# Performance work log

Measured on AMD Instinct MI355X. Metric: run time of the kernel, lower is better.

## Reference

```python
import jax, jax.numpy as jnp
import numpy as np

B, N, D_IN, D_H, D_OUT = 32768, 8, 256, 512, 256
LN_EPS = 1e-5


def setup_inputs() -> dict:
    key = jax.random.key(0)
    ks = jax.random.split(key, 9)
    s = lambda fan_in: 1.0 / np.sqrt(fan_in)
    return {
        "state": jax.random.normal(ks[0], (B, D_IN), dtype=jnp.float32),
        "neighbor_states": jax.random.normal(ks[1], (N, B, D_IN), dtype=jnp.float32),
        "ln_gamma": jnp.ones((D_IN,), jnp.float32),
        "ln_beta": jnp.zeros((D_IN,), jnp.float32),
        "W1": jax.random.uniform(ks[2], (D_IN, D_H), jnp.float32, -s(D_IN), s(D_IN)),
        "b1": jax.random.uniform(ks[3], (D_H,), jnp.float32, -s(D_IN), s(D_IN)),
        "W2": jax.random.uniform(ks[4], (D_H, D_OUT), jnp.float32, -s(D_H), s(D_H)),
        "b2": jax.random.uniform(ks[5], (D_OUT,), jnp.float32, -s(D_H), s(D_H)),
        "attn_w": jax.random.uniform(ks[6], (D_OUT,), jnp.float32, -s(D_OUT), s(D_OUT)),
        "attn_b": jax.random.uniform(ks[7], (), jnp.float32, -s(D_OUT), s(D_OUT)),
    }


def reference(state, neighbor_states, ln_gamma, ln_beta, W1, b1, W2, b2, attn_w, attn_b):
    def process(x):
        # LayerNorm over last dim (eps=1e-5, elementwise affine)
        mu = jnp.mean(x, axis=-1, keepdims=True)
        var = jnp.mean(jnp.square(x - mu), axis=-1, keepdims=True)
        xn = (x - mu) * jax.lax.rsqrt(var + LN_EPS) * ln_gamma + ln_beta
        # Linear -> (Dropout=identity in eval) -> ReLU -> Linear
        h = jax.nn.relu(xn @ W1 + b1)
        return h @ W2 + b2

    local = process(state)                      # [B, D_OUT]
    nf = process(neighbor_states)               # [N, B, D_OUT]
    # attention aggregation: scores over neighbor axis (torch stacks at dim=1)
    scores = jnp.einsum("nbo,o->nb", nf, attn_w) + attn_b   # [N, B]
    weights = jax.nn.softmax(scores, axis=0)                  # softmax over neighbors
    agg = jnp.einsum("nbo,nb->bo", nf, weights)              # [B, D_OUT]
    return local + agg
```

## Files before the change

kernel.cpp:

```cpp
#include <hip/hip_runtime.h>
#include <hip/hip_bf16.h>
#include <math.h>

#define BROWS 32768
#define NNB   8
#define DIN   256
#define DH    512
#define DOUT  256
#define MTILE 64
#define CH    32
#define NCHUNK 16
#define SA    264
#define SH    40

typedef __attribute__((ext_vector_type(8))) short bfrag;
typedef __attribute__((ext_vector_type(4))) float ffrag;
typedef __attribute__((ext_vector_type(4))) short s4v;

__device__ __forceinline__ short f2bf(float f) {
    union { float f; unsigned u; } v; v.f = f;
    unsigned r = v.u + 0x7fffu + ((v.u >> 16) & 1u);
    return (short)(r >> 16);
}

__global__ void tcast(const float* __restrict__ src, short* __restrict__ dst,
                      int R, int C) {
    __shared__ short t[64][67];
    const int c0 = blockIdx.x * 64, r0 = blockIdx.y * 64;
    const int lr = threadIdx.x >> 6, lc = threadIdx.x & 63;
    #pragma unroll
    for (int i = 0; i < 16; ++i) {
        int row = i * 4 + lr;
        t[row][lc] = f2bf(src[(size_t)(r0 + row) * C + c0 + lc]);
    }
    __syncthreads();
    #pragma unroll
    for (int i = 0; i < 16; ++i) {
        int row = i * 4 + lr;
        dst[(size_t)(c0 + row) * R + r0 + lc] = t[lc][row];
    }
}

__global__ __launch_bounds__(256, 2)
void fused_node(const float* __restrict__ state, const float* __restrict__ nbr,
                const float* __restrict__ gamma, const float* __restrict__ beta,
                const float* __restrict__ b1g, const float* __restrict__ b2g,
                const float* __restrict__ awg, const float* __restrict__ abg,
                const short* __restrict__ w1t, const short* __restrict__ w2t,
                float* __restrict__ out) {
    __shared__ short xn_lds[MTILE * SA];
    __shared__ short w1_lds[CH * SA];
    __shared__ short w2_lds[DOUT * SH];
    __shared__ short h_lds[MTILE * SH];
    __shared__ float g_lds[DIN], bt_lds[DIN];
    __shared__ float scorep[4 * MTILE];
    __shared__ float m_lds[MTILE], l_lds[MTILE], al_lds[MTILE], pp_lds[MTILE], il_lds[MTILE];

    const int tid = threadIdx.x;
    const int wv = tid >> 6, lane = tid & 63;
    const int q = lane >> 4, l16 = lane & 15;
    const int row0 = blockIdx.x * MTILE;
    const int cb = wv * 64;

    g_lds[tid] = gamma[tid];
    bt_lds[tid] = beta[tid];
    if (tid < MTILE) { m_lds[tid] = -__builtin_huge_valf(); l_lds[tid] = 0.f; }

    float b2v[4], awv[4];
    #pragma unroll
    for (int ct = 0; ct < 4; ++ct) {
        int col = cb + ct * 16 + l16;
        b2v[ct] = b2g[col];
        awv[ct] = awg[col];
    }
    const float attnb = abg[0];

    ffrag agg[4][4];
    #pragma unroll
    for (int mt = 0; mt < 4; ++mt)
        #pragma unroll
        for (int ct = 0; ct < 4; ++ct) {
            ffrag z = {0.f, 0.f, 0.f, 0.f};
            agg[mt][ct] = z;
        }

    ffrag feat[4][4];

    for (int s = 0; s < 9; ++s) {
        const bool loc = (s == 8);
        const float* xb = loc ? (state + (size_t)row0 * DIN)
                              : (nbr + ((size_t)s * BROWS + (size_t)row0) * DIN);
        __syncthreads();
        {
            const int r = tid >> 2, qq = tid & 3;
            const float* src = xb + r * DIN + qq * 64;
            float s0 = 0.f, s1 = 0.f, q0 = 0.f, q1 = 0.f;
            #pragma unroll
            for (int i = 0; i < 16; ++i) {
                float4 v = ((const float4*)src)[i];
                s0 += v.x + v.y;
                s1 += v.z + v.w;
                q0 = fmaf(v.x, v.x, fmaf(v.y, v.y, q0));
                q1 = fmaf(v.z, v.z, fmaf(v.w, v.w, q1));
            }
            float sum = s0 + s1, ssq = q0 + q1;
            sum += __shfl_xor(sum, 1); sum += __shfl_xor(sum, 2);
            ssq += __shfl_xor(ssq, 1); ssq += __shfl_xor(ssq, 2);
            float mean = sum * (1.f / 256.f);
            float var = ssq * (1.f / 256.f) - mean * mean;
            float rstd = rsqrtf(var + 1e-5f);
            short* dst = xn_lds + r * SA + qq * 64;
            #pragma unroll
            for (int i = 0; i < 16; ++i) {
                float4 v = ((const float4*)src)[i];
                int c = qq * 64 + i * 4;
                float4 g4 = *(const float4*)(g_lds + c);
                float4 t4 = *(const float4*)(bt_lds + c);
                s4v t;
                t.x = f2bf(fmaf((v.x - mean) * rstd, g4.x, t4.x));
                t.y = f2bf(fmaf((v.y - mean) * rstd, g4.y, t4.y));
                t.z = f2bf(fmaf((v.z - mean) * rstd, g4.z, t4.z));
                t.w = f2bf(fmaf((v.w - mean) * rstd, g4.w, t4.w));
                *(s4v*)(dst + i * 4) = t;
            }
        }
        #pragma unroll
        for (int mt = 0; mt < 4; ++mt)
            #pragma unroll
            for (int ct = 0; ct < 4; ++ct) {
                ffrag fi = {b2v[ct], b2v[ct], b2v[ct], b2v[ct]};
                feat[mt][ct] = fi;
            }

        for (int c = 0; c < NCHUNK; ++c) {
            __syncthreads();
            {
                const short* s1 = w1t + c * CH * DIN;
                #pragma unroll
                for (int i = 0; i < 4; ++i) {
                    int f = tid + 256 * i;
                    int rr = f >> 5, c8 = f & 31;
                    *(bfrag*)(w1_lds + rr * SA + c8 * 8) = *(const bfrag*)(s1 + f * 8);
                }
                const short* s2 = w2t + c * CH;
                #pragma unroll
                for (int i = 0; i < 4; ++i) {
                    int f = tid + 256 * i;
                    int rr = f >> 2, c8 = f & 3;
                    *(bfrag*)(w2_lds + rr * SH + c8 * 8) = *(const bfrag*)(s2 + rr * DH + c8 * 8);
                }
            }
            __syncthreads();
            {
                float bb0 = b1g[c * CH + l16], bb1 = b1g[c * CH + 16 + l16];
                ffrag h0 = {bb0, bb0, bb0, bb0};
                ffrag h1 = {bb1, bb1, bb1, bb1};
                const short* ap  = xn_lds + (wv * 16 + l16) * SA + q * 8;
                const short* bp0 = w1_lds + l16 * SA + q * 8;
                const short* bp1 = w1_lds + (16 + l16) * SA + q * 8;
                #pragma unroll
                for (int kb = 0; kb < 8; ++kb) {
                    bfrag a  = *(const bfrag*)(ap + kb * 32);
                    bfrag v0 = *(const bfrag*)(bp0 + kb * 32);
                    bfrag v1 = *(const bfrag*)(bp1 + kb * 32);
                    h0 = __builtin_amdgcn_mfma_f32_16x16x32_bf16(a, v0, h0, 0, 0, 0);
                    h1 = __builtin_amdgcn_mfma_f32_16x16x32_bf16(a, v1, h1, 0, 0, 0);
                }
                short* hb = h_lds + (wv * 16 + q * 4) * SH + l16;
                #pragma unroll
                for (int r = 0; r < 4; ++r) {
                    hb[r * SH]      = f2bf(fmaxf(h0[r], 0.f));
                    hb[r * SH + 16] = f2bf(fmaxf(h1[r], 0.f));
                }
            }
            __syncthreads();
            {
                bfrag af[4], bf[4];
                #pragma unroll
                for (int mt = 0; mt < 4; ++mt)
                    af[mt] = *(const bfrag*)(h_lds + (mt * 16 + l16) * SH + q * 8);
                #pragma unroll
                for (int ct = 0; ct < 4; ++ct)
                    bf[ct] = *(const bfrag*)(w2_lds + (cb + ct * 16 + l16) * SH + q * 8);
                #pragma unroll
                for (int mt = 0; mt < 4; ++mt)
                    #pragma unroll
                    for (int ct = 0; ct < 4; ++ct)
                        feat[mt][ct] = __builtin_amdgcn_mfma_f32_16x16x32_bf16(af[mt], bf[ct], feat[mt][ct], 0, 0, 0);
            }
        }

        if (!loc) {
            float sp[4][4];
            #pragma unroll
            for (int mt = 0; mt < 4; ++mt)
                #pragma unroll
                for (int r = 0; r < 4; ++r) {
                    float vv = feat[mt][0][r] * awv[0] + feat[mt][1][r] * awv[1]
                             + feat[mt][2][r] * awv[2] + feat[mt][3][r] * awv[3];
                    vv += __shfl_xor(vv, 1); vv += __shfl_xor(vv, 2);
                    vv += __shfl_xor(vv, 4); vv += __shfl_xor(vv, 8);
                    sp[mt][r] = vv;
                }
            if (l16 == 0) {
                #pragma unroll
                for (int mt = 0; mt < 4; ++mt)
                    #pragma unroll
                    for (int r = 0; r < 4; ++r)
                        scorep[wv * MTILE + mt * 16 + q * 4 + r] = sp[mt][r];
            }
            __syncthreads();
            if (tid < MTILE) {
                float sc = scorep[tid] + scorep[MTILE + tid] + scorep[2 * MTILE + tid]
                         + scorep[3 * MTILE + tid] + attnb;
                float mo = m_lds[tid];
                float mn = fmaxf(mo, sc);
                float al = __expf(mo - mn);
                float pp = __expf(sc - mn);
                float ln = l_lds[tid] * al + pp;
                m_lds[tid] = mn; l_lds[tid] = ln;
                al_lds[tid] = al; pp_lds[tid] = pp;
                if (s == NNB - 1) il_lds[tid] = 1.f / ln;
            }
            __syncthreads();
            #pragma unroll
            for (int mt = 0; mt < 4; ++mt) {
                float alv[4], ppv[4];
                #pragma unroll
                for (int r = 0; r < 4; ++r) {
                    int rr = mt * 16 + q * 4 + r;
                    alv[r] = al_lds[rr]; ppv[r] = pp_lds[rr];
                }
                #pragma unroll
                for (int ct = 0; ct < 4; ++ct)
                    #pragma unroll
                    for (int r = 0; r < 4; ++r)
                        agg[mt][ct][r] = agg[mt][ct][r] * alv[r] + ppv[r] * feat[mt][ct][r];
            }
        }
    }

    #pragma unroll
    for (int mt = 0; mt < 4; ++mt)
        #pragma unroll
        for (int r = 0; r < 4; ++r) {
            int rr = mt * 16 + q * 4 + r;
            float il = il_lds[rr];
            size_t base = (size_t)(row0 + rr) * DOUT + cb + l16;
            #pragma unroll
            for (int ct = 0; ct < 4; ++ct)
                out[base + ct * 16] = feat[mt][ct][r] + agg[mt][ct][r] * il;
        }
}

extern "C" void kernel_launch(void* const* d_in, const int* in_sizes, int n_in,
                              void* d_out, int out_size, void* d_ws, size_t ws_size,
                              hipStream_t stream) {
    const float* state = (const float*)d_in[0];
    const float* nbr   = (const float*)d_in[1];
    const float* gamma = (const float*)d_in[2];
    const float* beta  = (const float*)d_in[3];
    const float* W1    = (const float*)d_in[4];
    const float* b1    = (const float*)d_in[5];
    const float* W2    = (const float*)d_in[6];
    const float* b2    = (const float*)d_in[7];
    const float* aw    = (const float*)d_in[8];
    const float* ab    = (const float*)d_in[9];
    float* out = (float*)d_out;

    short* w1t = (short*)d_ws;
    short* w2t = w1t + (size_t)DH * DIN;

    tcast<<<dim3(DH / 64, DIN / 64), 256, 0, stream>>>(W1, w1t, DIN, DH);
    tcast<<<dim3(DOUT / 64, DH / 64), 256, 0, stream>>>(W2, w2t, DH, DOUT);
    fused_node<<<BROWS / MTILE, 256, 0, stream>>>(state, nbr, gamma, beta,
                                                  b1, b2, aw, ab, w1t, w2t, out);
}
```

Measured before the change: 723.2 us.

## Double-buffer weight chunks, fold LayerNorm affine into W1, keep xn in registers

Folds the LayerNorm gamma into W1 and beta into a precomputed b1, which removes the affine work from the hot loop. The normalized activations now live in registers as MFMA A-fragments instead of LDS. The block grows to 512 threads and 128 rows, and W1/W2 chunks are double-buffered with register prefetch to overlap global loads with compute and remove one barrier per chunk. Nontemporal loads and stores are added for the streaming activations and output. In exchange the kernel uses more registers per thread and launches a few extra small kernels.

Result: faster. 635.4 us (-12.1%).

```diff
diff --git a/kernel.cpp b/kernel.cpp
--- a/kernel.cpp
+++ b/kernel.cpp
@@ -7,7 +7,7 @@
 #define DIN   256
 #define DH    512
 #define DOUT  256
-#define MTILE 64
+#define MROWS 128
 #define CH    32
 #define NCHUNK 16
 #define SA    264
@@ -15,12 +15,30 @@
 
 typedef __attribute__((ext_vector_type(8))) short bfrag;
 typedef __attribute__((ext_vector_type(4))) float ffrag;
-typedef __attribute__((ext_vector_type(4))) short s4v;
+typedef __attribute__((ext_vector_type(4))) float f4v;
 
 __device__ __forceinline__ short f2bf(float f) {
     union { float f; unsigned u; } v; v.f = f;
     unsigned r = v.u + 0x7fffu + ((v.u >> 16) & 1u);
     return (short)(r >> 16);
+}
+
+__global__ void tcast_g(const float* __restrict__ src, const float* __restrict__ g,
+                        short* __restrict__ dst, int R, int C) {
+    __shared__ short t[64][67];
+    const int c0 = blockIdx.x * 64, r0 = blockIdx.y * 64;
+    const int lr = threadIdx.x >> 6, lc = threadIdx.x & 63;
+    #pragma unroll
+    for (int i = 0; i < 16; ++i) {
+        int row = i * 4 + lr;
+        t[row][lc] = f2bf(src[(size_t)(r0 + row) * C + c0 + lc] * g[r0 + row]);
+    }
+    __syncthreads();
+    #pragma unroll
+    for (int i = 0; i < 16; ++i) {
+        int row = i * 4 + lr;
+        dst[(size_t)(c0 + row) * R + r0 + lc] = t[lc][row];
+    }
 }
 
 __global__ void tcast(const float* __restrict__ src, short* __restrict__ dst,
@@ -41,35 +59,53 @@
     }
 }
 
-__global__ __launch_bounds__(256, 2)
+__global__ void b1prep(const float* __restrict__ W1, const float* __restrict__ b1,
+                       const float* __restrict__ beta, float* __restrict__ b1p) {
+    int n = blockIdx.x * 256 + threadIdx.x;
+    float acc = b1[n];
+    for (int k = 0; k < DIN; ++k) acc += beta[k] * W1[(size_t)k * DH + n];
+    b1p[n] = acc;
+}
+
+__global__ __launch_bounds__(512, 2)
 void fused_node(const float* __restrict__ state, const float* __restrict__ nbr,
-                const float* __restrict__ gamma, const float* __restrict__ beta,
-                const float* __restrict__ b1g, const float* __restrict__ b2g,
+                const float* __restrict__ b1p, const float* __restrict__ b2g,
                 const float* __restrict__ awg, const float* __restrict__ abg,
                 const short* __restrict__ w1t, const short* __restrict__ w2t,
                 float* __restrict__ out) {
-    __shared__ short xn_lds[MTILE * SA];
-    __shared__ short w1_lds[CH * SA];
-    __shared__ short w2_lds[DOUT * SH];
-    __shared__ short h_lds[MTILE * SH];
-    __shared__ float g_lds[DIN], bt_lds[DIN];
-    __shared__ float scorep[4 * MTILE];
-    __shared__ float m_lds[MTILE], l_lds[MTILE], al_lds[MTILE], pp_lds[MTILE], il_lds[MTILE];
+    __shared__ short w1_lds[2][CH * SA];
+    __shared__ short w2_lds[2][DOUT * SH];
+    __shared__ short h_lds[MROWS * SH];
+    __shared__ float b1_lds[DH];
+    __shared__ float scorep[4 * MROWS];
+    __shared__ float m_lds[MROWS], l_lds[MROWS], al_lds[MROWS], pp_lds[MROWS], il_lds[MROWS];
 
     const int tid = threadIdx.x;
     const int wv = tid >> 6, lane = tid & 63;
     const int q = lane >> 4, l16 = lane & 15;
-    const int row0 = blockIdx.x * MTILE;
-    const int cb = wv * 64;
-
-    g_lds[tid] = gamma[tid];
-    bt_lds[tid] = beta[tid];
-    if (tid < MTILE) { m_lds[tid] = -__builtin_huge_valf(); l_lds[tid] = 0.f; }
+    const int rg = wv >> 2, cg = wv & 3;
+    const int row0 = blockIdx.x * MROWS;
+    const int myrow = 16 * wv + l16;
+
+    const int f0 = tid, f1 = tid + 512;
+    const int w1r0 = f0 >> 5, w1c0 = f0 & 31, w1r1 = f1 >> 5, w1c1 = f1 & 31;
+    const int w2r0 = f0 >> 2, w2c0 = f0 & 3,  w2r1 = f1 >> 2, w2c1 = f1 & 3;
+
+    bfrag L1a = *(const bfrag*)(w1t + (size_t)f0 * 8);
+    bfrag L1b = *(const bfrag*)(w1t + (size_t)f1 * 8);
+    bfrag L2a = *(const bfrag*)(w2t + (size_t)w2r0 * DH + w2c0 * 8);
+    bfrag L2b = *(const bfrag*)(w2t + (size_t)w2r1 * DH + w2c1 * 8);
+    if (tid < DH) b1_lds[tid] = b1p[tid];
+    if (tid < MROWS) { m_lds[tid] = -__builtin_huge_valf(); l_lds[tid] = 0.f; }
+    *(bfrag*)(&w1_lds[0][w1r0 * SA + w1c0 * 8]) = L1a;
+    *(bfrag*)(&w1_lds[0][w1r1 * SA + w1c1 * 8]) = L1b;
+    *(bfrag*)(&w2_lds[0][w2r0 * SH + w2c0 * 8]) = L2a;
+    *(bfrag*)(&w2_lds[0][w2r1 * SH + w2c1 * 8]) = L2b;
 
     float b2v[4], awv[4];
     #pragma unroll
     for (int ct = 0; ct < 4; ++ct) {
-        int col = cb + ct * 16 + l16;
+        int col = 64 * cg + 16 * ct + l16;
         b2v[ct] = b2g[col];
         awv[ct] = awg[col];
     }
@@ -79,49 +115,46 @@
     #pragma unroll
     for (int mt = 0; mt < 4; ++mt)
         #pragma unroll
-        for (int ct = 0; ct < 4; ++ct) {
-            ffrag z = {0.f, 0.f, 0.f, 0.f};
-            agg[mt][ct] = z;
-        }
+        for (int ct = 0; ct < 4; ++ct) { ffrag z = {0.f,0.f,0.f,0.f}; agg[mt][ct] = z; }
 
     ffrag feat[4][4];
+    bfrag xnf[8];
 
     for (int s = 0; s < 9; ++s) {
         const bool loc = (s == 8);
         const float* xb = loc ? (state + (size_t)row0 * DIN)
                               : (nbr + ((size_t)s * BROWS + (size_t)row0) * DIN);
-        __syncthreads();
         {
-            const int r = tid >> 2, qq = tid & 3;
-            const float* src = xb + r * DIN + qq * 64;
-            float s0 = 0.f, s1 = 0.f, q0 = 0.f, q1 = 0.f;
-            #pragma unroll
-            for (int i = 0; i < 16; ++i) {
-                float4 v = ((const float4*)src)[i];
-                s0 += v.x + v.y;
-                s1 += v.z + v.w;
-                q0 = fmaf(v.x, v.x, fmaf(v.y, v.y, q0));
-                q1 = fmaf(v.z, v.z, fmaf(v.w, v.w, q1));
-            }
-            float sum = s0 + s1, ssq = q0 + q1;
-            sum += __shfl_xor(sum, 1); sum += __shfl_xor(sum, 2);
-            ssq += __shfl_xor(ssq, 1); ssq += __shfl_xor(ssq, 2);
+            const float* xr = xb + (size_t)myrow * DIN + q * 8;
+            f4v xa[8], xc[8];
+            #pragma unroll
+            for (int kb = 0; kb < 8; ++kb) {
+                xa[kb] = __builtin_nontemporal_load((const f4v*)(xr + kb * 32));
+                xc[kb] = __builtin_nontemporal_load((const f4v*)(xr + kb * 32 + 4));
+            }
+            float sum = 0.f, ssq = 0.f;
+            #pragma unroll
+            for (int kb = 0; kb < 8; ++kb) {
+                #pragma unroll
+                for (int j = 0; j < 4; ++j) {
+                    sum += xa[kb][j] + xc[kb][j];
+                    ssq = fmaf(xa[kb][j], xa[kb][j], fmaf(xc[kb][j], xc[kb][j], ssq));
+                }
+            }
+            sum += __shfl_xor(sum, 16); sum += __shfl_xor(sum, 32);
+            ssq += __shfl_xor(ssq, 16); ssq += __shfl_xor(ssq, 32);
             float mean = sum * (1.f / 256.f);
             float var = ssq * (1.f / 256.f) - mean * mean;
             float rstd = rsqrtf(var + 1e-5f);
-            short* dst = xn_lds + r * SA + qq * 64;
-            #pragma unroll
-            for (int i = 0; i < 16; ++i) {
-                float4 v = ((const float4*)src)[i];
-                int c = qq * 64 + i * 4;
-                float4 g4 = *(const float4*)(g_lds + c);
-                float4 t4 = *(const float4*)(bt_lds + c);
-                s4v t;
-                t.x = f2bf(fmaf((v.x - mean) * rstd, g4.x, t4.x));
-                t.y = f2bf(fmaf((v.y - mean) * rstd, g4.y, t4.y));
-                t.z = f2bf(fmaf((v.z - mean) * rstd, g4.z, t4.z));
-                t.w = f2bf(fmaf((v.w - mean) * rstd, g4.w, t4.w));
-                *(s4v*)(dst + i * 4) = t;
+            #pragma unroll
+            for (int kb = 0; kb < 8; ++kb) {
+                bfrag t;
+                #pragma unroll
+                for (int j = 0; j < 4; ++j) {
+                    t[j]     = f2bf((xa[kb][j] - mean) * rstd);
+                    t[j + 4] = f2bf((xc[kb][j] - mean) * rstd);
+                }
+                xnf[kb] = t;
             }
         }
         #pragma unroll
@@ -133,60 +166,57 @@
             }
 
         for (int c = 0; c < NCHUNK; ++c) {
+            const int p = c & 1;
             __syncthreads();
+            const bool more = (c < NCHUNK - 1) || (s < 8);
+            const int nc = (c + 1) & (NCHUNK - 1);
+            if (more) {
+                const short* s1 = w1t + (size_t)nc * CH * DIN;
+                const short* s2 = w2t + nc * CH;
+                L1a = *(const bfrag*)(s1 + (size_t)f0 * 8);
+                L1b = *(const bfrag*)(s1 + (size_t)f1 * 8);
+                L2a = *(const bfrag*)(s2 + (size_t)w2r0 * DH + w2c0 * 8);
+                L2b = *(const bfrag*)(s2 + (size_t)w2r1 * DH + w2c1 * 8);
+            }
             {
-                const short* s1 = w1t + c * CH * DIN;
-                #pragma unroll
-                for (int i = 0; i < 4; ++i) {
-                    int f = tid + 256 * i;
-                    int rr = f >> 5, c8 = f & 31;
-                    *(bfrag*)(w1_lds + rr * SA + c8 * 8) = *(const bfrag*)(s1 + f * 8);
-                }
-                const short* s2 = w2t + c * CH;
-                #pragma unroll
-                for (int i = 0; i < 4; ++i) {
-                    int f = tid + 256 * i;
-                    int rr = f >> 2, c8 = f & 3;
-                    *(bfrag*)(w2_lds + rr * SH + c8 * 8) = *(const bfrag*)(s2 + rr * DH + c8 * 8);
-                }
-            }
-            __syncthreads();
-            {
-                float bb0 = b1g[c * CH + l16], bb1 = b1g[c * CH + 16 + l16];
+                float bb0 = b1_lds[c * CH + l16], bb1 = b1_lds[c * CH + 16 + l16];
                 ffrag h0 = {bb0, bb0, bb0, bb0};
                 ffrag h1 = {bb1, bb1, bb1, bb1};
-                const short* ap  = xn_lds + (wv * 16 + l16) * SA + q * 8;
-                const short* bp0 = w1_lds + l16 * SA + q * 8;
-                const short* bp1 = w1_lds + (16 + l16) * SA + q * 8;
+                const short* bp = &w1_lds[p][l16 * SA + q * 8];
                 #pragma unroll
                 for (int kb = 0; kb < 8; ++kb) {
-                    bfrag a  = *(const bfrag*)(ap + kb * 32);
-                    bfrag v0 = *(const bfrag*)(bp0 + kb * 32);
-                    bfrag v1 = *(const bfrag*)(bp1 + kb * 32);
-                    h0 = __builtin_amdgcn_mfma_f32_16x16x32_bf16(a, v0, h0, 0, 0, 0);
-                    h1 = __builtin_amdgcn_mfma_f32_16x16x32_bf16(a, v1, h1, 0, 0, 0);
-                }
-                short* hb = h_lds + (wv * 16 + q * 4) * SH + l16;
+                    bfrag v0 = *(const bfrag*)(bp + kb * 32);
+                    bfrag v1 = *(const bfrag*)(bp + 16 * SA + kb * 32);
+                    h0 = __builtin_amdgcn_mfma_f32_16x16x32_bf16(xnf[kb], v0, h0, 0, 0, 0);
+                    h1 = __builtin_amdgcn_mfma_f32_16x16x32_bf16(xnf[kb], v1, h1, 0, 0, 0);
+                }
+                short* hb = h_lds + (16 * wv + 4 * q) * SH + l16;
                 #pragma unroll
                 for (int r = 0; r < 4; ++r) {
                     hb[r * SH]      = f2bf(fmaxf(h0[r], 0.f));
                     hb[r * SH + 16] = f2bf(fmaxf(h1[r], 0.f));
                 }
             }
+            if (more) {
+                *(bfrag*)(&w1_lds[1 - p][w1r0 * SA + w1c0 * 8]) = L1a;
+                *(bfrag*)(&w1_lds[1 - p][w1r1 * SA + w1c1 * 8]) = L1b;
+                *(bfrag*)(&w2_lds[1 - p][w2r0 * SH + w2c0 * 8]) = L2a;
+                *(bfrag*)(&w2_lds[1 - p][w2r1 * SH + w2c1 * 8]) = L2b;
+            }
             __syncthreads();
             {
-                bfrag af[4], bf[4];
+                bfrag af[4], bfr[4];
                 #pragma unroll
                 for (int mt = 0; mt < 4; ++mt)
-                    af[mt] = *(const bfrag*)(h_lds + (mt * 16 + l16) * SH + q * 8);
+                    af[mt] = *(const bfrag*)(h_lds + (64 * rg + 16 * mt + l16) * SH + q * 8);
                 #pragma unroll
                 for (int ct = 0; ct < 4; ++ct)
-                    bf[ct] = *(const bfrag*)(w2_lds + (cb + ct * 16 + l16) * SH + q * 8);
+                    bfr[ct] = *(const bfrag*)(&w2_lds[p][(64 * cg + 16 * ct + l16) * SH + q * 8]);
                 #pragma unroll
                 for (int mt = 0; mt < 4; ++mt)
                     #pragma unroll
                     for (int ct = 0; ct < 4; ++ct)
-                        feat[mt][ct] = __builtin_amdgcn_mfma_f32_16x16x32_bf16(af[mt], bf[ct], feat[mt][ct], 0, 0, 0);
+                        feat[mt][ct] = __builtin_amdgcn_mfma_f32_16x16x32_bf16(af[mt], bfr[ct], feat[mt][ct], 0, 0, 0);
             }
         }
 
@@ -207,12 +237,12 @@
                 for (int mt = 0; mt < 4; ++mt)
                     #pragma unroll
                     for (int r = 0; r < 4; ++r)
-                        scorep[wv * MTILE + mt * 16 + q * 4 + r] = sp[mt][r];
+                        scorep[cg * MROWS + 64 * rg + 16 * mt + 4 * q + r] = sp[mt][r];
             }
             __syncthreads();
-            if (tid < MTILE) {
-                float sc = scorep[tid] + scorep[MTILE + tid] + scorep[2 * MTILE + tid]
-                         + scorep[3 * MTILE + tid] + attnb;
+            if (tid < MROWS) {
+                float sc = scorep[tid] + scorep[MROWS + tid] + scorep[2 * MROWS + tid]
+                         + scorep[3 * MROWS + tid] + attnb;
                 float mo = m_lds[tid];
                 float mn = fmaxf(mo, sc);
                 float al = __expf(mo - mn);
@@ -228,7 +258,7 @@
                 float alv[4], ppv[4];
                 #pragma unroll
                 for (int r = 0; r < 4; ++r) {
-                    int rr = mt * 16 + q * 4 + r;
+                    int rr = 64 * rg + 16 * mt + 4 * q + r;
                     alv[r] = al_lds[rr]; ppv[r] = pp_lds[rr];
                 }
                 #pragma unroll
@@ -244,12 +274,13 @@
     for (int mt = 0; mt < 4; ++mt)
         #pragma unroll
         for (int r = 0; r < 4; ++r) {
-            int rr = mt * 16 + q * 4 + r;
+            int rr = 64 * rg + 16 * mt + 4 * q + r;
             float il = il_lds[rr];
-            size_t base = (size_t)(row0 + rr) * DOUT + cb + l16;
+            size_t base = (size_t)(row0 + rr) * DOUT + 64 * cg + l16;
             #pragma unroll
             for (int ct = 0; ct < 4; ++ct)
-                out[base + ct * 16] = feat[mt][ct][r] + agg[mt][ct][r] * il;
+                __builtin_nontemporal_store(feat[mt][ct][r] + agg[mt][ct][r] * il,
+                                            out + base + ct * 16);
         }
 }
 
@@ -270,9 +301,11 @@
 
     short* w1t = (short*)d_ws;
     short* w2t = w1t + (size_t)DH * DIN;
-
-    tcast<<<dim3(DH / 64, DIN / 64), 256, 0, stream>>>(W1, w1t, DIN, DH);
+    float* b1p = (float*)(w2t + (size_t)DOUT * DH);
+
+    tcast_g<<<dim3(DH / 64, DIN / 64), 256, 0, stream>>>(W1, gamma, w1t, DIN, DH);
     tcast<<<dim3(DOUT / 64, DH / 64), 256, 0, stream>>>(W2, w2t, DH, DOUT);
-    fused_node<<<BROWS / MTILE, 256, 0, stream>>>(state, nbr, gamma, beta,
-                                                  b1, b2, aw, ab, w1t, w2t, out);
-}
+    b1prep<<<2, 256, 0, stream>>>(W1, b1, beta, b1p);
+    fused_node<<<BROWS / MROWS, 512, 0, stream>>>(state, nbr, b1p, b2, aw, ab,
+                                                  w1t, w2t, out);
+}
```
